# Kernel tuning notes

Measured on AMD Instinct MI355X. Metric: run time of the kernel, lower is better.

Reference implementation:

```python
import jax, jax.numpy as jnp
import numpy as np
from functools import partial

B, T, F = 4096, 256, 32
H1, H2, NT = 64, 32, 3


def _lstm_layer(x, W_ih, W_hh, b_ih, b_hh):
    """Torch-style LSTM (batch_first). x: [B,T,Fin], W_ih: [4H,Fin], W_hh: [4H,H].
    Gate order i, f, g, o. Returns all hidden states [B,T,H]."""
    Bsz = x.shape[0]
    H = W_hh.shape[1]
    # Precompute input contribution for all timesteps (one big GEMM)
    xg = jnp.einsum('btf,gf->btg', x, W_ih) + b_ih + b_hh  # [B,T,4H]

    def step(carry, xg_t):
        h, c = carry
        gates = xg_t + h @ W_hh.T  # [B,4H]
        i, f, g, o = jnp.split(gates, 4, axis=-1)
        i = jax.nn.sigmoid(i)
        f = jax.nn.sigmoid(f)
        g = jnp.tanh(g)
        o = jax.nn.sigmoid(o)
        c = f * c + i * g
        h = o * jnp.tanh(c)
        return (h, c), h

    init = (jnp.zeros((Bsz, H), x.dtype), jnp.zeros((Bsz, H), x.dtype))
    _, hs = jax.lax.scan(step, init, jnp.swapaxes(xg, 0, 1))  # hs: [T,B,H]
    return jnp.swapaxes(hs, 0, 1)


def setup_inputs() -> dict:
    key = jax.random.key(0)
    ks = jax.random.split(key, 12)
    s1 = 1.0 / np.sqrt(H1)
    s2 = 1.0 / np.sqrt(H2)
    u = lambda k, shape, s: jax.random.uniform(k, shape, jnp.float32, -s, s)
    return {
        'x': jax.random.normal(ks[0], (B, T, F), jnp.float32),
        'W_ih1': u(ks[1], (4 * H1, F), s1),
        'W_hh1': u(ks[2], (4 * H1, H1), s1),
        'b_ih1': u(ks[3], (4 * H1,), s1),
        'b_hh1': u(ks[4], (4 * H1,), s1),
        'W_ih2': u(ks[5], (4 * H2, H1), s2),
        'W_hh2': u(ks[6], (4 * H2, H2), s2),
        'b_ih2': u(ks[7], (4 * H2,), s2),
        'b_hh2': u(ks[8], (4 * H2,), s2),
        'W_head': u(ks[9], (NT, H2), s2),
        'b_head': u(ks[10], (NT,), s2),
    }


def reference(x, W_ih1, W_hh1, b_ih1, b_hh1, W_ih2, W_hh2, b_ih2, b_hh2, W_head, b_head):
    h1 = _lstm_layer(x, W_ih1, W_hh1, b_ih1, b_hh1)   # [B,T,64]; dropout is identity in eval
    h2 = _lstm_layer(h1, W_ih2, W_hh2, b_ih2, b_hh2)  # [B,T,32]
    last = h2[:, -1, :]                               # [B,32]
    return last @ W_head.T + b_head                   # [B,3]
```

## Files before the change

### kernel.cpp

```cpp
#include <hip/hip_runtime.h>

#define Bsz 4096
#define Tt  256
#define Ff  32
#define H1  64
#define H2  32
#define NTAPS 3
#define BT  8
#define NTHR 256
#define CH  16

typedef _Float16 half8  __attribute__((ext_vector_type(8)));
typedef __fp16   fp16x2 __attribute__((ext_vector_type(2)));
typedef float    f32x4  __attribute__((ext_vector_type(4)));

#define H1S 72
#define H2S 40
#define HDS 33

__device__ __forceinline__ float lstm_unit(float pi, float pf, float pg, float po,
                                           float& c) {
    const float K1 = 1.4426950408889634f;
    float ei = __builtin_amdgcn_exp2f(-K1 * pi);
    float ef = __builtin_amdgcn_exp2f(-K1 * pf);
    float eg = __builtin_amdgcn_exp2f(-2.0f * K1 * __builtin_fabsf(pg));
    float eo = __builtin_amdgcn_exp2f(-K1 * po);
    float f_ = __builtin_amdgcn_rcpf(1.0f + ef);
    float ig = (1.0f - eg) * __builtin_amdgcn_rcpf((1.0f + ei) * (1.0f + eg));
    ig = __builtin_copysignf(ig, pg);
    c = f_ * c + ig;
    float ec = __builtin_amdgcn_exp2f(-2.0f * K1 * __builtin_fabsf(c));
    float th = (1.0f - ec) * __builtin_amdgcn_rcpf((1.0f + eo) * (1.0f + ec));
    return __builtin_copysignf(th, c);
}

#define MFMA16(a, b, c) __builtin_amdgcn_mfma_f32_16x16x32_f16((a), (b), (c), 0, 0, 0)

__device__ __forceinline__ void dma16(const float* gp, const float* lp) {
    __builtin_amdgcn_global_load_lds(
        (const __attribute__((address_space(1))) void*)gp,
        (__attribute__((address_space(3))) void*)lp, 16, 0, 0);
}

__global__ __launch_bounds__(NTHR, 2)
void lstm2_fused(const float* __restrict__ x,
                 const float* __restrict__ Wih1, const float* __restrict__ Whh1,
                 const float* __restrict__ bih1, const float* __restrict__ bhh1,
                 const float* __restrict__ Wih2, const float* __restrict__ Whh2,
                 const float* __restrict__ bih2, const float* __restrict__ bhh2,
                 const float* __restrict__ Whead, const float* __restrict__ bhead,
                 float* __restrict__ out)
{
    __shared__ __align__(16) _Float16 sH1[2][BT][H1S];
    __shared__ __align__(16) _Float16 sH2[2][BT][H2S];
    __shared__ __align__(16) float    sXC[2][CH][8][8][4];
    __shared__ __align__(16) float    sHead[BT][HDS];

    const int tid  = threadIdx.x;
    const int wid  = tid >> 6;
    const int lane = tid & 63;
    const int l15  = lane & 15;
    const int q    = lane >> 4;
    const int row8 = l15 & 7;
    const int b0   = blockIdx.x * BT;

    const int colL1 = wid * 16 + l15;
    const int r0  = (q >> 1) * 2, r1 = r0 + 1;
    const int bLo = (q & 1) * 4 + (q >> 1) * 2;
    const int hT   = wid >> 1, wpar = wid & 1;
    const int hL2  = hT * 16 + l15;
    const int rL2  = 2 * wpar + (q >> 1);
    const int bL2  = (q & 1) * 4 + 2 * wpar + (q >> 1);

    const int bL  = lane & 7;
    const int f4L = lane >> 3;
    const float* gbase = x + (size_t)(b0 + bL) * Tt * Ff + f4L * 4;

    #pragma unroll
    for (int j = 0; j < 4; ++j) {
        int t = (wid << 2) | j;
        dma16(gbase + (size_t)t * Ff, &sXC[0][t][0][0][0]);
    }

    half8 w1[4][3], w2[4][3];
    float bias1[4], bias2[4];
    #pragma unroll
    for (int G = 0; G < 4; ++G) {
        int gr1 = G * 64 + wid * 16 + l15;
        int gr2 = G * 32 + hT * 16 + l15;
        #pragma unroll
        for (int c = 0; c < 3; ++c) {
            half8 v1, v2;
            #pragma unroll
            for (int e = 0; e < 8; ++e) {
                int k = c * 32 + q * 8 + e;
                float f1 = (k < H1) ? Whh1[gr1 * H1 + k] : Wih1[gr1 * Ff + (k - H1)];
                int kk = q * 8 + e;
                float f2 = (c == 0) ? Whh2[gr2 * H2 + kk]
                                    : Wih2[gr2 * H1 + (c - 1) * 32 + kk];
                v1[e] = (_Float16)f1; v2[e] = (_Float16)f2;
            }
            w1[G][c] = v1; w2[G][c] = v2;
        }
        bias1[G] = bih1[gr1] + bhh1[gr1];
        bias2[G] = bih2[gr2] + bhh2[gr2];
    }

    for (int idx = tid; idx < BT * H1S; idx += NTHR) ((_Float16*)sH1[1])[idx] = (_Float16)0.0f;
    for (int idx = tid; idx < BT * H2S; idx += NTHR) ((_Float16*)sH2[1])[idx] = (_Float16)0.0f;

    __syncthreads();

    float cs0 = 0.0f, cs1 = 0.0f, cs2 = 0.0f;

    for (int i = 0; i <= Tt; ++i) {
        const int cur = i & 1, nxt = cur ^ 1;
        const int t16 = i & (CH - 1), cbuf = (i >> 4) & 1;

        half8 a0 = *(const half8*)&sH1[nxt][row8][q * 8];
        half8 a1 = *(const half8*)&sH1[nxt][row8][32 + q * 8];

        if (i < Tt) {
            f32x4 lo = *(const f32x4*)&sXC[cbuf][t16][2 * q][row8][0];
            f32x4 hi = *(const f32x4*)&sXC[cbuf][t16][2 * q + 1][row8][0];
            union { half8 v; fp16x2 h[4]; } axu;
            axu.h[0] = __builtin_amdgcn_cvt_pkrtz(lo[0], lo[1]);
            axu.h[1] = __builtin_amdgcn_cvt_pkrtz(lo[2], lo[3]);
            axu.h[2] = __builtin_amdgcn_cvt_pkrtz(hi[0], hi[1]);
            axu.h[3] = __builtin_amdgcn_cvt_pkrtz(hi[2], hi[3]);

            f32x4 acc[4];
            #pragma unroll
            for (int G = 0; G < 4; ++G) {
                f32x4 a = {bias1[G], bias1[G], bias1[G], bias1[G]};
                a = MFMA16(a0, w1[G][0], a);
                a = MFMA16(a1, w1[G][1], a);
                a = MFMA16(axu.v, w1[G][2], a);
                acc[G] = a;
            }
            float h0  = lstm_unit(acc[0][r0], acc[1][r0], acc[2][r0], acc[3][r0], cs0);
            float h1v = lstm_unit(acc[0][r1], acc[1][r1], acc[2][r1], acc[3][r1], cs1);
            sH1[cur][bLo][colL1]     = (_Float16)h0;
            sH1[cur][bLo + 1][colL1] = (_Float16)h1v;
        }
        if (i >= 1) {
            half8 ah = *(const half8*)&sH2[cur][row8][q * 8];
            f32x4 acc[4];
            #pragma unroll
            for (int G = 0; G < 4; ++G) {
                f32x4 a = {bias2[G], bias2[G], bias2[G], bias2[G]};
                a = MFMA16(ah, w2[G][0], a);
                a = MFMA16(a0, w2[G][1], a);
                a = MFMA16(a1, w2[G][2], a);
                acc[G] = a;
            }
            float h2v = lstm_unit(acc[0][rL2], acc[1][rL2], acc[2][rL2], acc[3][rL2], cs2);
            sH2[nxt][bL2][hL2] = (_Float16)h2v;
            if (i == Tt) sHead[bL2][hL2] = h2v;
        }

        if ((i & (CH - 1)) == 0 && i + CH < Tt) {
            const float* gb = gbase + (size_t)(i + CH) * Ff;
            #pragma unroll
            for (int j = 0; j < 4; ++j) {
                int t = (wid << 2) | j;
                dma16(gb + (size_t)t * Ff, &sXC[cbuf ^ 1][t][0][0][0]);
            }
        }
        __syncthreads();
    }

    if (tid < BT * NTAPS) {
        int b = tid / NTAPS, n = tid - b * NTAPS;
        float s = bhead[n];
        #pragma unroll
        for (int k = 0; k < H2; ++k) s = fmaf(sHead[b][k], Whead[n * H2 + k], s);
        out[(size_t)(b0 + b) * NTAPS + n] = s;
    }
}

extern "C" void kernel_launch(void* const* d_in, const int* in_sizes, int n_in,
                              void* d_out, int out_size, void* d_ws, size_t ws_size,
                              hipStream_t stream) {
    const float* xp    = (const float*)d_in[0];
    const float* Wih1  = (const float*)d_in[1];
    const float* Whh1  = (const float*)d_in[2];
    const float* bih1  = (const float*)d_in[3];
    const float* bhh1  = (const float*)d_in[4];
    const float* Wih2  = (const float*)d_in[5];
    const float* Whh2  = (const float*)d_in[6];
    const float* bih2  = (const float*)d_in[7];
    const float* bhh2  = (const float*)d_in[8];
    const float* Whead = (const float*)d_in[9];
    const float* bhead = (const float*)d_in[10];
    float* outp = (float*)d_out;

    hipLaunchKernelGGL(lstm2_fused, dim3(Bsz / BT), dim3(NTHR), 0, stream,
                       xp, Wih1, Whh1, bih1, bhh1, Wih2, Whh2, bih2, bhh2,
                       Whead, bhead, outp);
}
```

Before: 414.2 us.

## Split layer-1 and layer-2 LSTM work onto separate wavefronts per block

Doubles the block to 512 threads so waves 0-3 run only the layer-1 recurrence and waves 4-7 run only the layer-2 recurrence plus the x prefetch DMA. Each wave now holds one weight set instead of two, which lowers register pressure, and the two layers' MFMA and activation chains run concurrently rather than serially within a wave. The cost is twice as many threads per block sharing the same per-step barrier, which occupancy and register limits must still accommodate.

```diff
diff --git a/kernel.cpp b/kernel.cpp
--- a/kernel.cpp
+++ b/kernel.cpp
@@ -7,7 +7,7 @@
 #define H2  32
 #define NTAPS 3
 #define BT  8
-#define NTHR 256
+#define NTHR 512
 #define CH  16
 
 typedef _Float16 half8  __attribute__((ext_vector_type(8)));
@@ -42,7 +42,7 @@
         (__attribute__((address_space(3))) void*)lp, 16, 0, 0);
 }
 
-__global__ __launch_bounds__(NTHR, 2)
+__global__ __launch_bounds__(NTHR, 4)
 void lstm2_fused(const float* __restrict__ x,
                  const float* __restrict__ Wih1, const float* __restrict__ Whh1,
                  const float* __restrict__ bih1, const float* __restrict__ bhh1,
@@ -63,11 +63,13 @@
     const int q    = lane >> 4;
     const int row8 = l15 & 7;
     const int b0   = blockIdx.x * BT;
-
-    const int colL1 = wid * 16 + l15;
+    const int w4   = wid & 3;
+    const bool isL1 = (wid < 4);
+
+    const int colL1 = w4 * 16 + l15;
     const int r0  = (q >> 1) * 2, r1 = r0 + 1;
     const int bLo = (q & 1) * 4 + (q >> 1) * 2;
-    const int hT   = wid >> 1, wpar = wid & 1;
+    const int hT   = w4 >> 1, wpar = w4 & 1;
     const int hL2  = hT * 16 + l15;
     const int rL2  = 2 * wpar + (q >> 1);
     const int bL2  = (q & 1) * 4 + 2 * wpar + (q >> 1);
@@ -76,34 +78,51 @@
     const int f4L = lane >> 3;
     const float* gbase = x + (size_t)(b0 + bL) * Tt * Ff + f4L * 4;
 
-    #pragma unroll
-    for (int j = 0; j < 4; ++j) {
-        int t = (wid << 2) | j;
-        dma16(gbase + (size_t)t * Ff, &sXC[0][t][0][0][0]);
-    }
-
-    half8 w1[4][3], w2[4][3];
-    float bias1[4], bias2[4];
-    #pragma unroll
-    for (int G = 0; G < 4; ++G) {
-        int gr1 = G * 64 + wid * 16 + l15;
-        int gr2 = G * 32 + hT * 16 + l15;
-        #pragma unroll
-        for (int c = 0; c < 3; ++c) {
-            half8 v1, v2;
-            #pragma unroll
-            for (int e = 0; e < 8; ++e) {
-                int k = c * 32 + q * 8 + e;
-                float f1 = (k < H1) ? Whh1[gr1 * H1 + k] : Wih1[gr1 * Ff + (k - H1)];
-                int kk = q * 8 + e;
-                float f2 = (c == 0) ? Whh2[gr2 * H2 + kk]
-                                    : Wih2[gr2 * H1 + (c - 1) * 32 + kk];
-                v1[e] = (_Float16)f1; v2[e] = (_Float16)f2;
-            }
-            w1[G][c] = v1; w2[G][c] = v2;
-        }
-        bias1[G] = bih1[gr1] + bhh1[gr1];
-        bias2[G] = bih2[gr2] + bhh2[gr2];
+    if (!isL1) {
+        #pragma unroll
+        for (int j = 0; j < 4; ++j) {
+            int t = (w4 << 2) | j;
+            dma16(gbase + (size_t)t * Ff, &sXC[0][t][0][0][0]);
+        }
+    }
+
+    half8 w[4][3];
+    float bias[4];
+    if (isL1) {
+        #pragma unroll
+        for (int G = 0; G < 4; ++G) {
+            int gr = G * 64 + w4 * 16 + l15;
+            #pragma unroll
+            for (int c = 0; c < 3; ++c) {
+                half8 v;
+                #pragma unroll
+                for (int e = 0; e < 8; ++e) {
+                    int k = c * 32 + q * 8 + e;
+                    float f = (k < H1) ? Whh1[gr * H1 + k] : Wih1[gr * Ff + (k - H1)];
+                    v[e] = (_Float16)f;
+                }
+                w[G][c] = v;
+            }
+            bias[G] = bih1[gr] + bhh1[gr];
+        }
+    } else {
+        #pragma unroll
+        for (int G = 0; G < 4; ++G) {
+            int gr = G * 32 + hT * 16 + l15;
+            #pragma unroll
+            for (int c = 0; c < 3; ++c) {
+                half8 v;
+                #pragma unroll
+                for (int e = 0; e < 8; ++e) {
+                    int kk = q * 8 + e;
+                    float f = (c == 0) ? Whh2[gr * H2 + kk]
+                                       : Wih2[gr * H1 + (c - 1) * 32 + kk];
+                    v[e] = (_Float16)f;
+                }
+                w[G][c] = v;
+            }
+            bias[G] = bih2[gr] + bhh2[gr];
+        }
     }
 
     for (int idx = tid; idx < BT * H1S; idx += NTHR) ((_Float16*)sH1[1])[idx] = (_Float16)0.0f;
@@ -111,62 +130,64 @@
 
     __syncthreads();
 
-    float cs0 = 0.0f, cs1 = 0.0f, cs2 = 0.0f;
+    float csA = 0.0f, csB = 0.0f;
 
     for (int i = 0; i <= Tt; ++i) {
         const int cur = i & 1, nxt = cur ^ 1;
         const int t16 = i & (CH - 1), cbuf = (i >> 4) & 1;
 
+        if (!isL1 && t16 == 0 && i + CH < Tt) {
+            const float* gb = gbase + (size_t)(i + CH) * Ff;
+            #pragma unroll
+            for (int j = 0; j < 4; ++j) {
+                int t = (w4 << 2) | j;
+                dma16(gb + (size_t)t * Ff, &sXC[cbuf ^ 1][t][0][0][0]);
+            }
+        }
+
         half8 a0 = *(const half8*)&sH1[nxt][row8][q * 8];
         half8 a1 = *(const half8*)&sH1[nxt][row8][32 + q * 8];
 
-        if (i < Tt) {
-            f32x4 lo = *(const f32x4*)&sXC[cbuf][t16][2 * q][row8][0];
-            f32x4 hi = *(const f32x4*)&sXC[cbuf][t16][2 * q + 1][row8][0];
-            union { half8 v; fp16x2 h[4]; } axu;
-            axu.h[0] = __builtin_amdgcn_cvt_pkrtz(lo[0], lo[1]);
-            axu.h[1] = __builtin_amdgcn_cvt_pkrtz(lo[2], lo[3]);
-            axu.h[2] = __builtin_amdgcn_cvt_pkrtz(hi[0], hi[1]);
-            axu.h[3] = __builtin_amdgcn_cvt_pkrtz(hi[2], hi[3]);
-
-            f32x4 acc[4];
-            #pragma unroll
-            for (int G = 0; G < 4; ++G) {
-                f32x4 a = {bias1[G], bias1[G], bias1[G], bias1[G]};
-                a = MFMA16(a0, w1[G][0], a);
-                a = MFMA16(a1, w1[G][1], a);
-                a = MFMA16(axu.v, w1[G][2], a);
-                acc[G] = a;
-            }
-            float h0  = lstm_unit(acc[0][r0], acc[1][r0], acc[2][r0], acc[3][r0], cs0);
-            float h1v = lstm_unit(acc[0][r1], acc[1][r1], acc[2][r1], acc[3][r1], cs1);
-            sH1[cur][bLo][colL1]     = (_Float16)h0;
-            sH1[cur][bLo + 1][colL1] = (_Float16)h1v;
-        }
-        if (i >= 1) {
+        if (isL1) {
+            if (i < Tt) {
+                f32x4 lo = *(const f32x4*)&sXC[cbuf][t16][2 * q][row8][0];
+                f32x4 hi = *(const f32x4*)&sXC[cbuf][t16][2 * q + 1][row8][0];
+                union { half8 v; fp16x2 h[4]; } axu;
+                axu.h[0] = __builtin_amdgcn_cvt_pkrtz(lo[0], lo[1]);
+                axu.h[1] = __builtin_amdgcn_cvt_pkrtz(lo[2], lo[3]);
+                axu.h[2] = __builtin_amdgcn_cvt_pkrtz(hi[0], hi[1]);
+                axu.h[3] = __builtin_amdgcn_cvt_pkrtz(hi[2], hi[3]);
+
+                f32x4 acc[4];
+                #pragma unroll
+                for (int G = 0; G < 4; ++G) {
+                    f32x4 a = {bias[G], bias[G], bias[G], bias[G]};
+                    a = MFMA16(a0, w[G][0], a);
+                    a = MFMA16(a1, w[G][1], a);
+                    a = MFMA16(axu.v, w[G][2], a);
+                    acc[G] = a;
+                }
+                float h0  = lstm_unit(acc[0][r0], acc[1][r0], acc[2][r0], acc[3][r0], csA);
+                float h1v = lstm_unit(acc[0][r1], acc[1][r1], acc[2][r1], acc[3][r1], csB);
+                sH1[cur][bLo][colL1]     = (_Float16)h0;
+                sH1[cur][bLo + 1][colL1] = (_Float16)h1v;
+            }
+        } else if (i >= 1) {
             half8 ah = *(const half8*)&sH2[cur][row8][q * 8];
             f32x4 acc[4];
             #pragma unroll
             for (int G = 0; G < 4; ++G) {
-                f32x4 a = {bias2[G], bias2[G], bias2[G], bias2[G]};
-                a = MFMA16(ah, w2[G][0], a);
-                a = MFMA16(a0, w2[G][1], a);
-                a = MFMA16(a1, w2[G][2], a);
+                f32x4 a = {bias[G], bias[G], bias[G], bias[G]};
+                a = MFMA16(ah, w[G][0], a);
+                a = MFMA16(a0, w[G][1], a);
+                a = MFMA16(a1, w[G][2], a);
                 acc[G] = a;
             }
-            float h2v = lstm_unit(acc[0][rL2], acc[1][rL2], acc[2][rL2], acc[3][rL2], cs2);
+            float h2v = lstm_unit(acc[0][rL2], acc[1][rL2], acc[2][rL2], acc[3][rL2], csA);
             sH2[nxt][bL2][hL2] = (_Float16)h2v;
             if (i == Tt) sHead[bL2][hL2] = h2v;
         }
 
-        if ((i & (CH - 1)) == 0 && i + CH < Tt) {
-            const float* gb = gbase + (size_t)(i + CH) * Ff;
-            #pragma unroll
-            for (int j = 0; j < 4; ++j) {
-                int t = (wid << 2) | j;
-                dma16(gb + (size_t)t * Ff, &sXC[cbuf ^ 1][t][0][0][0]);
-            }
-        }
         __syncthreads();
     }
 
```

New measurement: 410.3 us. No clear change (-0.9%).
